# Optimization experiments

Measured on AMD Instinct MI355X. Metric: run time of the kernel, lower is better.

## Reference

```python
import jax, jax.numpy as jnp
import numpy as np

B, L, HID, NH, HD = 2, 2048, 1024, 16, 64


def _positions_and_segs(lengths):
    # lengths: (L,) int64, sub-sequence lengths packed at front, zeros pad.
    cs = jnp.cumsum(lengths)                       # (L,) segment end offsets
    t = jnp.arange(lengths.shape[0])
    seg = jnp.searchsorted(cs, t, side='right')    # segment id per token
    seg = jnp.minimum(seg, lengths.shape[0] - 1)
    starts = cs - lengths                          # segment start offsets
    pos = t - starts[seg]                          # position reset per segment
    valid = t < cs[-1]
    return jnp.where(valid, pos, 0), seg, valid


def _rope(x, positions):
    # x: (B, L, H, D); positions: (B, L)
    d = x.shape[-1]
    inv_freq = 1.0 / (10000.0 ** (jnp.arange(0, d, 2, dtype=jnp.float32) / d))
    freqs = positions[..., None].astype(jnp.float32) * inv_freq   # (B, L, d/2)
    emb = jnp.concatenate([freqs, freqs], axis=-1)                # (B, L, d)
    cos = jnp.cos(emb)[:, :, None, :]
    sin = jnp.sin(emb)[:, :, None, :]
    x1, x2 = jnp.split(x, 2, axis=-1)
    rot = jnp.concatenate([-x2, x1], axis=-1)
    return x * cos + rot * sin


def setup_inputs() -> dict:
    key = jax.random.key(0)
    ks = jax.random.split(key, 5)
    hidden_states = jax.random.normal(ks[0], (B, L, HID), dtype=jnp.float32)
    aml = np.zeros((B, L), dtype=np.int64)
    aml[0, :3] = [512, 768, 520]    # sums to 1800 (248 padding tokens)
    aml[1, :3] = [1024, 512, 512]   # sums to 2048 (no padding)
    attention_mask_in_length = jnp.asarray(aml)
    Wqkv = jax.random.normal(ks[1], (HID, 3 * HID), dtype=jnp.float32) * 0.02
    bqkv = jax.random.normal(ks[2], (3 * HID,), dtype=jnp.float32) * 0.02
    Wout = jax.random.normal(ks[3], (HID, HID), dtype=jnp.float32) * 0.02
    bout = jax.random.normal(ks[4], (HID,), dtype=jnp.float32) * 0.02
    return {"hidden_states": hidden_states,
            "attention_mask_in_length": attention_mask_in_length,
            "Wqkv": Wqkv, "bqkv": bqkv, "Wout": Wout, "bout": bout}


def reference(hidden_states, attention_mask_in_length, Wqkv, bqkv, Wout, bout):
    Bb, Ll, _ = hidden_states.shape
    qkv = hidden_states @ Wqkv + bqkv                 # (B, L, 3*HID)
    qkv = qkv.reshape(Bb, Ll, 3, NH, HD)
    q, k, v = qkv[:, :, 0], qkv[:, :, 1], qkv[:, :, 2]
    scale = HD ** -0.5
    q = q * scale  # module pre-scales q before RoPE
    positions, seg, valid = jax.vmap(_positions_and_segs)(attention_mask_in_length)
    q = _rope(q, positions)
    k = _rope(k, positions)
    # block-diagonal attention: only within same sub-sequence, valid tokens
    mask = (seg[:, :, None] == seg[:, None, :]) & valid[:, :, None] & valid[:, None, :]
    # flash_attn with softmax_scale=None applies head_dim**-0.5 again (faithful)
    scores = jnp.einsum('bihd,bjhd->bhij', q, k) * scale
    scores = jnp.where(mask[:, None, :, :], scores, -1e9)
    probs = jax.nn.softmax(scores, axis=-1)
    out = jnp.einsum('bhij,bjhd->bihd', probs, v)     # (B, L, H, D)
    out = jnp.where(valid[:, :, None, None], out, 0.0)  # pad_input zeros padding rows
    out = out.reshape(Bb, Ll, NH * HD)
    return out @ Wout + bout
```

## Files before the change

kernel.cpp:

```cpp
#include <hip/hip_runtime.h>
#include <math.h>

#define B_ 2
#define L_ 2048
#define HID_ 1024
#define NH_ 16
#define HD_ 64
#define QBLK 128

typedef unsigned short u16;
typedef __attribute__((ext_vector_type(8))) _Float16 half8;
typedef __attribute__((ext_vector_type(4))) float f32x4;

__device__ __forceinline__ u16 f2h(float x) {
    _Float16 h = (_Float16)x; u16 r; __builtin_memcpy(&r, &h, 2); return r;
}
__device__ __forceinline__ float fexp2(float x) {
    float r;
    asm("v_exp_f32 %0, %1" : "=v"(r) : "v"(x));
    return r;
}
__device__ __forceinline__ unsigned pkrtz(float a, float b) {
    auto v = __builtin_amdgcn_cvt_pkrtz(a, b);
    unsigned r; __builtin_memcpy(&r, &v, 4); return r;
}
__device__ __forceinline__ void gload16(const void* g, void* l) {
    __builtin_amdgcn_global_load_lds(
        (const __attribute__((address_space(1))) void*)g,
        (__attribute__((address_space(3))) void*)l, 16, 0, 0);
}

__global__ void setup_kernel(const int* __restrict__ aml,
                             int* __restrict__ sstart, int* __restrict__ send,
                             int* __restrict__ poss_out)
{
    const int b = blockIdx.x;
    const int tid = threadIdx.x;
    __shared__ int cs[L_];
    __shared__ int partial[256];

    int vals[8];
    const int t0 = tid * 8;
    int s = 0;
#pragma unroll
    for (int e = 0; e < 8; ++e) { vals[e] = aml[b * L_ + t0 + e]; s += vals[e]; }
    partial[tid] = s;
    __syncthreads();
    if (tid == 0) {
        int acc = 0;
        for (int i = 0; i < 256; ++i) { int tmp = partial[i]; partial[i] = acc; acc += tmp; }
    }
    __syncthreads();
    int off = partial[tid];
#pragma unroll
    for (int e = 0; e < 8; ++e) { off += vals[e]; cs[t0 + e] = off; }
    __syncthreads();

    const int total = cs[L_ - 1];
    for (int t = tid; t < L_; t += 256) {
        int lo = 0, hi = L_;
        while (lo < hi) { int mid = (lo + hi) >> 1; if (cs[mid] <= t) lo = mid + 1; else hi = mid; }
        int seg = lo < (L_ - 1) ? lo : (L_ - 1);
        int end = cs[seg];
        int len = aml[b * L_ + seg];
        int start = end - len;
        bool valid = t < total;
        poss_out[b * L_ + t] = valid ? (t - start) : 0;
        sstart[b * L_ + t] = valid ? start : 0x7fffffff;
        send[b * L_ + t]   = valid ? end : 0;
    }
}

__global__ void conv_all(const float* __restrict__ hidden, u16* __restrict__ hidh,
                         const float* __restrict__ Wqkv, u16* __restrict__ wqh,
                         const float* __restrict__ Wout, u16* __restrict__ woh,
                         const int* __restrict__ poss,
                         float* __restrict__ ctab, float* __restrict__ stab)
{
    __shared__ float t[32][33];
    const int bid = blockIdx.x;
    const int tid = threadIdx.x;
    if (bid < 4096) {
        int i = (bid * 256 + tid) * 4;
        float4 v = *(const float4*)&hidden[i];
        *(ushort4*)&hidh[i] = make_ushort4(f2h(v.x), f2h(v.y), f2h(v.z), f2h(v.w));
        return;
    }
    if (bid >= 8192) {
        const double kexp = 13.287712379549449 / 32.0;
        int idx = (bid - 8192) * 256 + tid;
        int d = idx & 31;
        int bt = idx >> 5;
        double f = (double)poss[bt] * exp2(-(double)d * kexp);
        ctab[idx] = (float)cos(f);
        stab[idx] = (float)sin(f);
        return;
    }
    const float* W; u16* o; int Kd = 1024, Nd, n0, k0;
    if (bid < 7168) {
        int idx = bid - 4096; W = Wqkv; o = wqh; Nd = 3072;
        n0 = (idx % 96) * 32; k0 = (idx / 96) * 32;
    } else {
        int idx = bid - 7168; W = Wout; o = woh; Nd = 1024;
        n0 = (idx & 31) * 32; k0 = (idx >> 5) * 32;
    }
    const int r = tid >> 5, c = tid & 31;
#pragma unroll
    for (int i = 0; i < 4; ++i)
        t[r + 8 * i][c] = W[(size_t)(k0 + r + 8 * i) * Nd + n0 + c];
    __syncthreads();
#pragma unroll
    for (int i = 0; i < 4; ++i)
        o[(size_t)(n0 + r + 8 * i) * Kd + k0 + c] = f2h(t[c][r + 8 * i]);
}

template <int MODE>
__global__ __launch_bounds__(256, 3)
void gemm_mfma(const u16* __restrict__ Ap, const u16* __restrict__ Bp,
               const float* __restrict__ bias, float* __restrict__ C,
               u16* __restrict__ qb, u16* __restrict__ kb, u16* __restrict__ vtb,
               const float* __restrict__ ctab, const float* __restrict__ stab,
               int M, int N, int K)
{
    __shared__ u16 Asl[128 * 64];
    __shared__ u16 Bsl[128 * 64];

    const int tid = threadIdx.x;
    const int wave = tid >> 6, lane = tid & 63;

    const int nwg = gridDim.x * gridDim.y;
    const int bid = blockIdx.y * gridDim.x + blockIdx.x;
    const int cpx = nwg >> 3;
    const int swz = (bid & 7) * cpx + (bid >> 3);
    const int brow = (swz / gridDim.x) * 128;
    const int bcol = (swz % gridDim.x) * 128;

    const int wr = (wave >> 1) * 64, wc = (wave & 1) * 64;
    const int grow = tid >> 3, gslot = tid & 7;
    const int fr = lane & 15, kg = lane >> 4;

    f32x4 acc[4][4];
#pragma unroll
    for (int m = 0; m < 4; ++m)
#pragma unroll
        for (int n = 0; n < 4; ++n) acc[m][n] = (f32x4){0.f, 0.f, 0.f, 0.f};

    for (int ka = 0; ka < K; ka += 64) {
#pragma unroll
        for (int c = 0; c < 4; ++c) {
            int row = c * 32 + grow;
            int sg = gslot ^ (row & 7);
            gload16(&Ap[(size_t)(brow + row) * K + ka + sg * 8],
                    (char*)Asl + c * 4096 + wave * 1024);
            gload16(&Bp[(size_t)(bcol + row) * K + ka + sg * 8],
                    (char*)Bsl + c * 4096 + wave * 1024);
        }
        __syncthreads();

#pragma unroll
        for (int kk = 0; kk < 2; ++kk) {
            half8 af[4], bfv[4];
            const int cbase = kk * 4 + kg;
#pragma unroll
            for (int n = 0; n < 4; ++n) {
                int r = wc + n * 16 + fr;
                bfv[n] = *(const half8*)&Bsl[r * 64 + ((cbase ^ (r & 7)) << 3)];
            }
#pragma unroll
            for (int m = 0; m < 4; ++m) {
                int r = wr + m * 16 + fr;
                af[m] = *(const half8*)&Asl[r * 64 + ((cbase ^ (r & 7)) << 3)];
            }
#pragma unroll
            for (int m = 0; m < 4; ++m)
#pragma unroll
                for (int n = 0; n < 4; ++n)
                    acc[m][n] = __builtin_amdgcn_mfma_f32_16x16x32_f16(
                        af[m], bfv[n], acc[m][n], 0, 0, 0);
        }
        __syncthreads();
    }

    const int cr = (lane >> 4) * 4;
    const int cc = lane & 15;
    if (MODE == 0) {
#pragma unroll
        for (int m = 0; m < 4; ++m) {
#pragma unroll
            for (int n = 0; n < 4; ++n) {
                const int col = bcol + wc + n * 16 + cc;
                const float bv = bias[col];
                const int row0 = brow + wr + m * 16 + cr;
#pragma unroll
                for (int rg = 0; rg < 4; ++rg)
                    C[(size_t)(row0 + rg) * N + col] = acc[m][n][rg] + bv;
            }
        }
    } else {
        const int colbase = bcol + wc;
        const int sel = colbase >> 10;
        const int hh = (colbase & 1023) >> 6;
#pragma unroll
        for (int m = 0; m < 4; ++m) {
            const int row0 = brow + wr + m * 16 + cr;
            const int bidx = row0 >> 11, t0 = row0 & (L_ - 1);
            if (sel == 2) {
#pragma unroll
                for (int n = 0; n < 4; ++n) {
                    int col = colbase + n * 16 + cc;
                    float bv = bias[col];
                    int d = col & 63;
                    ushort4 pk = make_ushort4(
                        f2h(acc[m][n][0] + bv), f2h(acc[m][n][1] + bv),
                        f2h(acc[m][n][2] + bv), f2h(acc[m][n][3] + bv));
                    *(ushort4*)&vtb[((((size_t)bidx * NH_ + hh) * HD_) + d) * L_ + t0] = pk;
                }
            } else {
                u16* dst = (sel == 0) ? qb : kb;
#pragma unroll
                for (int np = 0; np < 2; ++np) {
                    int col1 = colbase + np * 16 + cc;
                    int d1 = np * 16 + cc;
                    float bv1 = bias[col1], bv2 = bias[col1 + 32];
#pragma unroll
                    for (int rg = 0; rg < 4; ++rg) {
                        int t = t0 + rg;
                        float c = ctab[((size_t)bidx * L_ + t) * 32 + d1];
                        float s = stab[((size_t)bidx * L_ + t) * 32 + d1];
                        float x1 = acc[m][np][rg] + bv1;
                        float x2 = acc[m][np + 2][rg] + bv2;
                        size_t base = ((((size_t)bidx * NH_ + hh) * L_) + t) * (size_t)HD_;
                        dst[base + d1]      = f2h(x1 * c - x2 * s);
                        dst[base + d1 + 32] = f2h(x2 * c + x1 * s);
                    }
                }
            }
        }
    }
}

__global__ __launch_bounds__(512)
void attn_mfma(const u16* __restrict__ qb, const u16* __restrict__ kbuf,
               const u16* __restrict__ vt, const int* __restrict__ sstart,
               const int* __restrict__ send, u16* __restrict__ ohi)
{
    __shared__ u16 Ksb[3][64 * 64];
    __shared__ u16 Vsb[3][64 * 64];
    __shared__ u16 Pw[8 * 16 * 64];
    __shared__ int ss[QBLK], se[QBLK];

    const int b = blockIdx.z, h = blockIdx.y, q0 = blockIdx.x * QBLK;
    const int tid = threadIdx.x, wave = tid >> 6, lane = tid & 63;
    const int fr = lane & 15, kg = lane >> 4;
    const size_t hb = (((size_t)b * NH_) + h) * (size_t)(L_ * HD_);
    const size_t hv = (((size_t)b * NH_) + h) * (size_t)(HD_ * L_);

    if (tid < QBLK) { ss[tid] = sstart[b * L_ + q0 + tid]; se[tid] = send[b * L_ + q0 + tid]; }

    const u16* qrow = &qb[hb + (size_t)(q0 + wave * 16 + fr) * HD_ + kg * 8];
    half8 qf0 = *(const half8*)(qrow);
    half8 qf1 = *(const half8*)(qrow + 32);
    __syncthreads();

    int kmin = 0x7fffffff, kmax = 0;
#pragma unroll 8
    for (int r = 0; r < QBLK; ++r) { kmin = min(kmin, ss[r]); kmax = max(kmax, se[r]); }

    const int myss_ = ss[wave * 16 + fr];
    const int myse_ = se[wave * 16 + fr];

    float l_ = 0.f;
    f32x4 oacc[4];
#pragma unroll
    for (int i = 0; i < 4; ++i) oacc[i] = (f32x4){0.f, 0.f, 0.f, 0.f};

    const int grow = tid >> 3;
    const int sg = (tid & 7) ^ (grow & 7);
    const float SCL = 0.015625f * 1.4426950408889634f;
    const int fx = fr & 7;
    u16* pwl = &Pw[wave * 1024 + fr * 64];

    const int kt_first = kmin & ~63;
    const int ntile = (kmax > kt_first) ? ((kmax - kt_first + 63) >> 6) : 0;

    if (ntile > 0) {
        gload16(&kbuf[hb + (size_t)(kt_first + grow) * HD_ + sg * 8],
                (char*)Ksb[0] + wave * 1024);
        gload16(&vt[hv + (size_t)grow * L_ + kt_first + sg * 8],
                (char*)Vsb[0] + wave * 1024);
    }
    if (ntile > 1) {
        gload16(&kbuf[hb + (size_t)(kt_first + 64 + grow) * HD_ + sg * 8],
                (char*)Ksb[1] + wave * 1024);
        gload16(&vt[hv + (size_t)grow * L_ + kt_first + 64 + sg * 8],
                (char*)Vsb[1] + wave * 1024);
    }
    __syncthreads();

    for (int i = 0; i < ntile; ++i) {
        const int kt0 = kt_first + i * 64;

        if (i + 1 < ntile) {
            asm volatile("s_waitcnt vmcnt(2)" ::: "memory");
        } else {
            asm volatile("s_waitcnt vmcnt(0)" ::: "memory");
        }
        __builtin_amdgcn_sched_barrier(0);
        __builtin_amdgcn_s_barrier();

        if (i + 2 < ntile) {
            const int ktn = kt0 + 128;
            gload16(&kbuf[hb + (size_t)(ktn + grow) * HD_ + sg * 8],
                    (char*)Ksb[(i + 2) % 3] + wave * 1024);
            gload16(&vt[hv + (size_t)grow * L_ + ktn + sg * 8],
                    (char*)Vsb[(i + 2) % 3] + wave * 1024);
        }

        const u16* Ks = Ksb[i % 3];
        const u16* Vs = Vsb[i % 3];

        f32x4 sc4[4];
#pragma unroll
        for (int ct = 0; ct < 4; ++ct) sc4[ct] = (f32x4){0.f, 0.f, 0.f, 0.f};
        __builtin_amdgcn_s_setprio(1);
#pragma unroll
        for (int kk = 0; kk < 2; ++kk) {
            half8 qf = kk ? qf1 : qf0;
#pragma unroll
            for (int ct = 0; ct < 4; ++ct) {
                int r = ct * 16 + fr;
                half8 kf = *(const half8*)&Ks[r * 64 + (((kk * 4 + kg) ^ (r & 7)) << 3)];
                sc4[ct] = __builtin_amdgcn_mfma_f32_16x16x32_f16(kf, qf, sc4[ct], 0, 0, 0);
            }
        }
        __builtin_amdgcn_s_setprio(0);

        float p[4][4];
        float psum = 0.f;
        if (__all((kt0 >= myss_) && (kt0 + 64 <= myse_))) {
#pragma unroll
            for (int ct = 0; ct < 4; ++ct)
#pragma unroll
                for (int reg = 0; reg < 4; ++reg) {
                    float e = fexp2(sc4[ct][reg] * SCL);
                    p[ct][reg] = e;
                    psum += e;
                }
        } else {
            const int ktb = kt0 + kg * 4;
#pragma unroll
            for (int ct = 0; ct < 4; ++ct)
#pragma unroll
                for (int reg = 0; reg < 4; ++reg) {
                    int kt = ktb + ct * 16 + reg;
                    bool v = (kt >= myss_) && (kt < myse_);
                    float e = fexp2(sc4[ct][reg] * SCL);
                    p[ct][reg] = v ? e : 0.f;
                    psum += p[ct][reg];
                }
        }
        psum += __shfl_xor(psum, 16);
        psum += __shfl_xor(psum, 32);
        l_ += psum;

#pragma unroll
        for (int ct = 0; ct < 4; ++ct) {
            uint2 w;
            w.x = pkrtz(p[ct][0], p[ct][1]);
            w.y = pkrtz(p[ct][2], p[ct][3]);
            *(uint2*)&pwl[(((2 * ct + (kg >> 1)) ^ fx) << 3) + (kg & 1) * 4] = w;
        }

        __builtin_amdgcn_s_setprio(1);
#pragma unroll
        for (int ks2 = 0; ks2 < 2; ++ks2) {
            half8 pf = *(const half8*)&pwl[((4 * ks2 + kg) ^ fx) << 3];
#pragma unroll
            for (int dt = 0; dt < 4; ++dt) {
                int r = dt * 16 + fr;
                half8 vf = *(const half8*)&Vs[r * 64 + (((ks2 * 4 + kg) ^ (r & 7)) << 3)];
                oacc[dt] = __builtin_amdgcn_mfma_f32_16x16x32_f16(vf, pf, oacc[dt], 0, 0, 0);
            }
        }
        __builtin_amdgcn_s_setprio(0);
    }

    const int t = q0 + wave * 16 + fr;
    const float inv = (myss_ < myse_) ? 1.f / l_ : 0.f;
    const size_t rowbase = ((size_t)b * L_ + t) * (size_t)HID_ + h * HD_ + kg * 4;
#pragma unroll
    for (int dt = 0; dt < 4; ++dt) {
        *(ushort4*)&ohi[rowbase + dt * 16] = make_ushort4(
            f2h(oacc[dt][0] * inv), f2h(oacc[dt][1] * inv),
            f2h(oacc[dt][2] * inv), f2h(oacc[dt][3] * inv));
    }
}

extern "C" void kernel_launch(void* const* d_in, const int* in_sizes, int n_in,
                              void* d_out, int out_size, void* d_ws, size_t ws_size,
                              hipStream_t stream)
{
    (void)in_sizes; (void)n_in; (void)out_size; (void)ws_size;
    const float* hidden = (const float*)d_in[0];
    const int*   aml    = (const int*)d_in[1];
    const float* Wqkv   = (const float*)d_in[2];
    const float* bqkv   = (const float*)d_in[3];
    const float* Wout   = (const float*)d_in[4];
    const float* bout   = (const float*)d_in[5];
    float* out = (float*)d_out;

    const size_t per = (size_t)B_ * NH_ * L_ * HD_;
    float* ctab = (float*)d_ws;
    float* stab = ctab + (size_t)B_ * L_ * 32;
    int* sstart = (int*)(stab + (size_t)B_ * L_ * 32);
    int* send   = sstart + B_ * L_;
    int* poss   = send + B_ * L_;
    u16* qbf  = (u16*)(poss + B_ * L_);
    u16* kbf  = qbf + per;
    u16* vtb  = kbf + per;
    u16* hidh = vtb + per;
    u16* wqh  = hidh + (size_t)4096 * 1024;
    u16* woh  = wqh + (size_t)3072 * 1024;

    setup_kernel<<<dim3(B_), dim3(256), 0, stream>>>(aml, sstart, send, poss);

    conv_all<<<dim3(8704), dim3(256), 0, stream>>>(hidden, hidh, Wqkv, wqh,
                                                   Wout, woh, poss, ctab, stab);

    gemm_mfma<1><<<dim3(24, 32), dim3(256), 0, stream>>>(
        hidh, wqh, bqkv, nullptr, qbf, kbf, vtb, ctab, stab,
        B_ * L_, 3 * HID_, HID_);

    attn_mfma<<<dim3(L_ / QBLK, NH_, B_), dim3(512), 0, stream>>>(
        qbf, kbf, vtb, sstart, send, hidh);

    gemm_mfma<0><<<dim3(8, 32), dim3(256), 0, stream>>>(
        hidh, woh, bout, out, nullptr, nullptr, nullptr, nullptr, nullptr,
        B_ * L_, HID_, HID_);
}
```

Measured before the change: 108.0 us.

## Rewrite attention kernel with 32x32x16 MFMA and register-resident P via lane shuffles

The attention kernel now runs 4 waves of 32 query rows each and uses 32x32x16 MFMA instead of 16x16x32, which increases per-wave reuse of K/V fragments. The probability tile no longer goes through an LDS scratch buffer; it is repacked in registers with cross-half lane shuffles to form the B operand. The K/V pipeline drops from triple buffering with vmcnt waits to double buffering with a full barrier per tile. This gives fewer LDS reads per MFMA but more registers per thread, and the prefetch depth is shorter.

```diff
diff --git a/kernel.cpp b/kernel.cpp
--- a/kernel.cpp
+++ b/kernel.cpp
@@ -11,6 +11,7 @@
 typedef unsigned short u16;
 typedef __attribute__((ext_vector_type(8))) _Float16 half8;
 typedef __attribute__((ext_vector_type(4))) float f32x4;
+typedef __attribute__((ext_vector_type(16))) float f32x16;
 
 __device__ __forceinline__ u16 f2h(float x) {
     _Float16 h = (_Float16)x; u16 r; __builtin_memcpy(&r, &h, 2); return r;
@@ -239,161 +240,170 @@
     }
 }
 
-__global__ __launch_bounds__(512)
+__global__ __launch_bounds__(256)
 void attn_mfma(const u16* __restrict__ qb, const u16* __restrict__ kbuf,
                const u16* __restrict__ vt, const int* __restrict__ sstart,
                const int* __restrict__ send, u16* __restrict__ ohi)
 {
-    __shared__ u16 Ksb[3][64 * 64];
-    __shared__ u16 Vsb[3][64 * 64];
-    __shared__ u16 Pw[8 * 16 * 64];
+    __shared__ u16 Ksb[2][64 * 64];
+    __shared__ u16 Vsb[2][64 * 64];
     __shared__ int ss[QBLK], se[QBLK];
 
     const int b = blockIdx.z, h = blockIdx.y, q0 = blockIdx.x * QBLK;
     const int tid = threadIdx.x, wave = tid >> 6, lane = tid & 63;
-    const int fr = lane & 15, kg = lane >> 4;
+    const int l31 = lane & 31, hi = lane >> 5;
     const size_t hb = (((size_t)b * NH_) + h) * (size_t)(L_ * HD_);
     const size_t hv = (((size_t)b * NH_) + h) * (size_t)(HD_ * L_);
 
     if (tid < QBLK) { ss[tid] = sstart[b * L_ + q0 + tid]; se[tid] = send[b * L_ + q0 + tid]; }
 
-    const u16* qrow = &qb[hb + (size_t)(q0 + wave * 16 + fr) * HD_ + kg * 8];
-    half8 qf0 = *(const half8*)(qrow);
-    half8 qf1 = *(const half8*)(qrow + 32);
+    const u16* qptr = &qb[hb + (size_t)(q0 + wave * 32 + l31) * HD_ + hi * 8];
+    half8 qf[4];
+#pragma unroll
+    for (int s = 0; s < 4; ++s) qf[s] = *(const half8*)(qptr + s * 16);
     __syncthreads();
 
     int kmin = 0x7fffffff, kmax = 0;
 #pragma unroll 8
     for (int r = 0; r < QBLK; ++r) { kmin = min(kmin, ss[r]); kmax = max(kmax, se[r]); }
 
-    const int myss_ = ss[wave * 16 + fr];
-    const int myse_ = se[wave * 16 + fr];
+    const int myss_ = ss[wave * 32 + l31];
+    const int myse_ = se[wave * 32 + l31];
 
     float l_ = 0.f;
-    f32x4 oacc[4];
-#pragma unroll
-    for (int i = 0; i < 4; ++i) oacc[i] = (f32x4){0.f, 0.f, 0.f, 0.f};
+    f32x16 oacc[2];
+#pragma unroll
+    for (int i = 0; i < 16; ++i) { oacc[0][i] = 0.f; oacc[1][i] = 0.f; }
 
     const int grow = tid >> 3;
     const int sg = (tid & 7) ^ (grow & 7);
     const float SCL = 0.015625f * 1.4426950408889634f;
-    const int fx = fr & 7;
-    u16* pwl = &Pw[wave * 1024 + fr * 64];
+    const int fx = l31 & 7;
 
     const int kt_first = kmin & ~63;
     const int ntile = (kmax > kt_first) ? ((kmax - kt_first + 63) >> 6) : 0;
 
     if (ntile > 0) {
-        gload16(&kbuf[hb + (size_t)(kt_first + grow) * HD_ + sg * 8],
-                (char*)Ksb[0] + wave * 1024);
-        gload16(&vt[hv + (size_t)grow * L_ + kt_first + sg * 8],
-                (char*)Vsb[0] + wave * 1024);
-    }
-    if (ntile > 1) {
-        gload16(&kbuf[hb + (size_t)(kt_first + 64 + grow) * HD_ + sg * 8],
-                (char*)Ksb[1] + wave * 1024);
-        gload16(&vt[hv + (size_t)grow * L_ + kt_first + 64 + sg * 8],
-                (char*)Vsb[1] + wave * 1024);
-    }
-    __syncthreads();
-
+#pragma unroll
+        for (int c = 0; c < 2; ++c) {
+            int row = c * 32 + grow;
+            gload16(&kbuf[hb + (size_t)(kt_first + row) * HD_ + sg * 8],
+                    (char*)Ksb[0] + c * 4096 + wave * 1024);
+            gload16(&vt[hv + (size_t)row * L_ + kt_first + sg * 8],
+                    (char*)Vsb[0] + c * 4096 + wave * 1024);
+        }
+    }
+    __syncthreads();
+
+    int bufi = 0;
     for (int i = 0; i < ntile; ++i) {
         const int kt0 = kt_first + i * 64;
-
         if (i + 1 < ntile) {
-            asm volatile("s_waitcnt vmcnt(2)" ::: "memory");
-        } else {
-            asm volatile("s_waitcnt vmcnt(0)" ::: "memory");
-        }
-        __builtin_amdgcn_sched_barrier(0);
-        __builtin_amdgcn_s_barrier();
-
-        if (i + 2 < ntile) {
-            const int ktn = kt0 + 128;
-            gload16(&kbuf[hb + (size_t)(ktn + grow) * HD_ + sg * 8],
-                    (char*)Ksb[(i + 2) % 3] + wave * 1024);
-            gload16(&vt[hv + (size_t)grow * L_ + ktn + sg * 8],
-                    (char*)Vsb[(i + 2) % 3] + wave * 1024);
-        }
-
-        const u16* Ks = Ksb[i % 3];
-        const u16* Vs = Vsb[i % 3];
-
-        f32x4 sc4[4];
-#pragma unroll
-        for (int ct = 0; ct < 4; ++ct) sc4[ct] = (f32x4){0.f, 0.f, 0.f, 0.f};
+            const int ktn = kt0 + 64;
+#pragma unroll
+            for (int c = 0; c < 2; ++c) {
+                int row = c * 32 + grow;
+                gload16(&kbuf[hb + (size_t)(ktn + row) * HD_ + sg * 8],
+                        (char*)Ksb[bufi ^ 1] + c * 4096 + wave * 1024);
+                gload16(&vt[hv + (size_t)row * L_ + ktn + sg * 8],
+                        (char*)Vsb[bufi ^ 1] + c * 4096 + wave * 1024);
+            }
+        }
+        const u16* Ks = Ksb[bufi];
+        const u16* Vs = Vsb[bufi];
+
+        f32x16 sc0, sc1;
+#pragma unroll
+        for (int r = 0; r < 16; ++r) { sc0[r] = 0.f; sc1[r] = 0.f; }
         __builtin_amdgcn_s_setprio(1);
 #pragma unroll
-        for (int kk = 0; kk < 2; ++kk) {
-            half8 qf = kk ? qf1 : qf0;
-#pragma unroll
-            for (int ct = 0; ct < 4; ++ct) {
-                int r = ct * 16 + fr;
-                half8 kf = *(const half8*)&Ks[r * 64 + (((kk * 4 + kg) ^ (r & 7)) << 3)];
-                sc4[ct] = __builtin_amdgcn_mfma_f32_16x16x32_f16(kf, qf, sc4[ct], 0, 0, 0);
-            }
+        for (int s = 0; s < 4; ++s) {
+            const int sl = (((s << 1) + hi) ^ fx) << 3;
+            half8 a0 = *(const half8*)&Ks[l31 * 64 + sl];
+            half8 a1 = *(const half8*)&Ks[(32 + l31) * 64 + sl];
+            sc0 = __builtin_amdgcn_mfma_f32_32x32x16_f16(a0, qf[s], sc0, 0, 0, 0);
+            sc1 = __builtin_amdgcn_mfma_f32_32x32x16_f16(a1, qf[s], sc1, 0, 0, 0);
         }
         __builtin_amdgcn_s_setprio(0);
 
-        float p[4][4];
         float psum = 0.f;
         if (__all((kt0 >= myss_) && (kt0 + 64 <= myse_))) {
 #pragma unroll
-            for (int ct = 0; ct < 4; ++ct)
-#pragma unroll
-                for (int reg = 0; reg < 4; ++reg) {
-                    float e = fexp2(sc4[ct][reg] * SCL);
-                    p[ct][reg] = e;
-                    psum += e;
-                }
+            for (int r = 0; r < 16; ++r) {
+                sc0[r] = fexp2(sc0[r] * SCL); psum += sc0[r];
+                sc1[r] = fexp2(sc1[r] * SCL); psum += sc1[r];
+            }
         } else {
-            const int ktb = kt0 + kg * 4;
-#pragma unroll
-            for (int ct = 0; ct < 4; ++ct)
-#pragma unroll
-                for (int reg = 0; reg < 4; ++reg) {
-                    int kt = ktb + ct * 16 + reg;
-                    bool v = (kt >= myss_) && (kt < myse_);
-                    float e = fexp2(sc4[ct][reg] * SCL);
-                    p[ct][reg] = v ? e : 0.f;
-                    psum += p[ct][reg];
-                }
-        }
-        psum += __shfl_xor(psum, 16);
+            const int ktb = kt0 + 4 * hi;
+#pragma unroll
+            for (int r = 0; r < 16; ++r) {
+                int key0 = ktb + (r & 3) + 8 * (r >> 2);
+                int key1 = key0 + 32;
+                bool v0 = (key0 >= myss_) && (key0 < myse_);
+                bool v1 = (key1 >= myss_) && (key1 < myse_);
+                float e0 = fexp2(sc0[r] * SCL);
+                float e1 = fexp2(sc1[r] * SCL);
+                sc0[r] = v0 ? e0 : 0.f; psum += sc0[r];
+                sc1[r] = v1 ? e1 : 0.f; psum += sc1[r];
+            }
+        }
         psum += __shfl_xor(psum, 32);
         l_ += psum;
 
-#pragma unroll
-        for (int ct = 0; ct < 4; ++ct) {
-            uint2 w;
-            w.x = pkrtz(p[ct][0], p[ct][1]);
-            w.y = pkrtz(p[ct][2], p[ct][3]);
-            *(uint2*)&pwl[(((2 * ct + (kg >> 1)) ^ fx) << 3) + (kg & 1) * 4] = w;
+        unsigned w0[4][2], w1[4][2], p0[4][2], p1[4][2];
+#pragma unroll
+        for (int g = 0; g < 4; ++g) {
+            w0[g][0] = pkrtz(sc0[4 * g + 0], sc0[4 * g + 1]);
+            w0[g][1] = pkrtz(sc0[4 * g + 2], sc0[4 * g + 3]);
+            w1[g][0] = pkrtz(sc1[4 * g + 0], sc1[4 * g + 1]);
+            w1[g][1] = pkrtz(sc1[4 * g + 2], sc1[4 * g + 3]);
+            p0[g][0] = __shfl_xor(w0[g][0], 32);
+            p0[g][1] = __shfl_xor(w0[g][1], 32);
+            p1[g][0] = __shfl_xor(w1[g][0], 32);
+            p1[g][1] = __shfl_xor(w1[g][1], 32);
         }
 
         __builtin_amdgcn_s_setprio(1);
 #pragma unroll
-        for (int ks2 = 0; ks2 < 2; ++ks2) {
-            half8 pf = *(const half8*)&pwl[((4 * ks2 + kg) ^ fx) << 3];
-#pragma unroll
-            for (int dt = 0; dt < 4; ++dt) {
-                int r = dt * 16 + fr;
-                half8 vf = *(const half8*)&Vs[r * 64 + (((ks2 * 4 + kg) ^ (r & 7)) << 3)];
-                oacc[dt] = __builtin_amdgcn_mfma_f32_16x16x32_f16(vf, pf, oacc[dt], 0, 0, 0);
+        for (int s = 0; s < 4; ++s) {
+            const int s1 = s & 1;
+            unsigned bw[4];
+            if ((s >> 1) == 0) {
+                bw[0] = hi ? p0[2 * s1 + 1][0] : w0[2 * s1][0];
+                bw[1] = hi ? p0[2 * s1 + 1][1] : w0[2 * s1][1];
+                bw[2] = hi ? w0[2 * s1 + 1][0] : p0[2 * s1][0];
+                bw[3] = hi ? w0[2 * s1 + 1][1] : p0[2 * s1][1];
+            } else {
+                bw[0] = hi ? p1[2 * s1 + 1][0] : w1[2 * s1][0];
+                bw[1] = hi ? p1[2 * s1 + 1][1] : w1[2 * s1][1];
+                bw[2] = hi ? w1[2 * s1 + 1][0] : p1[2 * s1][0];
+                bw[3] = hi ? w1[2 * s1 + 1][1] : p1[2 * s1][1];
+            }
+            half8 pf; __builtin_memcpy(&pf, bw, 16);
+            const int sl = (((s << 1) + hi) ^ fx) << 3;
+#pragma unroll
+            for (int dt = 0; dt < 2; ++dt) {
+                half8 vf = *(const half8*)&Vs[(dt * 32 + l31) * 64 + sl];
+                oacc[dt] = __builtin_amdgcn_mfma_f32_32x32x16_f16(vf, pf, oacc[dt], 0, 0, 0);
             }
         }
         __builtin_amdgcn_s_setprio(0);
-    }
-
-    const int t = q0 + wave * 16 + fr;
+        __syncthreads();
+        bufi ^= 1;
+    }
+
+    const int t = q0 + wave * 32 + l31;
     const float inv = (myss_ < myse_) ? 1.f / l_ : 0.f;
-    const size_t rowbase = ((size_t)b * L_ + t) * (size_t)HID_ + h * HD_ + kg * 4;
-#pragma unroll
-    for (int dt = 0; dt < 4; ++dt) {
-        *(ushort4*)&ohi[rowbase + dt * 16] = make_ushort4(
-            f2h(oacc[dt][0] * inv), f2h(oacc[dt][1] * inv),
-            f2h(oacc[dt][2] * inv), f2h(oacc[dt][3] * inv));
-    }
+    const size_t rowbase = ((size_t)b * L_ + t) * (size_t)HID_ + h * HD_;
+#pragma unroll
+    for (int dt = 0; dt < 2; ++dt)
+#pragma unroll
+        for (int g = 0; g < 4; ++g) {
+            ushort4 o = make_ushort4(
+                f2h(oacc[dt][4 * g + 0] * inv), f2h(oacc[dt][4 * g + 1] * inv),
+                f2h(oacc[dt][4 * g + 2] * inv), f2h(oacc[dt][4 * g + 3] * inv));
+            *(ushort4*)&ohi[rowbase + dt * 32 + 8 * g + 4 * hi] = o;
+        }
 }
 
 extern "C" void kernel_launch(void* const* d_in, const int* in_sizes, int n_in,
@@ -431,7 +441,7 @@
         hidh, wqh, bqkv, nullptr, qbf, kbf, vtb, ctab, stab,
         B_ * L_, 3 * HID_, HID_);
 
-    attn_mfma<<<dim3(L_ / QBLK, NH_, B_), dim3(512), 0, stream>>>(
+    attn_mfma<<<dim3(L_ / QBLK, NH_, B_), dim3(256), 0, stream>>>(
         qbf, kbf, vtb, sstart, send, hidh);
 
     gemm_mfma<0><<<dim3(8, 32), dim3(256), 0, stream>>>(
```

Measured after the change: 113.6 us. 1.05x slower.
